# Kernel optimization log

Hardware: AMD Instinct MI355X
Metric: run time of the kernel (lower is better)

Reference implementation:

```python
import jax, jax.numpy as jnp
import numpy as np

H = 128
H1 = H + 1          # 129
FUSE = H1 * H1 * H1 # 2,146,689


def setup_inputs() -> dict:
    key = jax.random.key(0)
    ks = jax.random.split(key, 9)
    B = 64
    v = jax.random.normal(ks[0], (B, H), dtype=jnp.float32)
    a = jax.random.normal(ks[1], (B, H), dtype=jnp.float32)
    t = jax.random.normal(ks[2], (B, H), dtype=jnp.float32)
    # Linear params stored as [in, out]; xavier-ish scaling
    W1 = jax.random.normal(ks[3], (FUSE, H // 2), dtype=jnp.float32) * (1.0 / np.sqrt(FUSE))
    b1 = jnp.zeros((H // 2,), dtype=jnp.float32)
    W2 = jax.random.normal(ks[4], (H // 2, H // 4), dtype=jnp.float32) * (1.0 / np.sqrt(H // 2))
    b2 = jnp.zeros((H // 4,), dtype=jnp.float32)
    W3 = jax.random.normal(ks[5], (H // 4, 1), dtype=jnp.float32) * (1.0 / np.sqrt(H // 4))
    b3 = jnp.zeros((1,), dtype=jnp.float32)
    return {"v": v, "a": a, "t": t, "W1": W1, "b1": b1,
            "W2": W2, "b2": b2, "W3": W3, "b3": b3}


def reference(v, a, t, W1, b1, W2, b2, W3, b3):
    B = a.shape[0]
    one = jnp.ones((B, 1), dtype=a.dtype)
    a_h = jnp.concatenate([one, a], axis=1)  # [B, H+1]
    v_h = jnp.concatenate([one, v], axis=1)
    t_h = jnp.concatenate([one, t], axis=1)
    # triple outer product: fusion[b,i,j,k] = a_h[b,i]*v_h[b,j]*t_h[b,k]
    fusion = jnp.einsum('bi,bj,bk->bijk', a_h, v_h, t_h).reshape(B, -1)  # [B, (H+1)^3]
    # dropout p applied at eval is identity (torch Dropout in eval / p=0)
    y1 = jax.nn.relu(fusion @ W1 + b1)
    y2 = jax.nn.relu(y1 @ W2 + b2)
    return y2 @ W3 + b3  # [B, 1]
```

## Files before the change

kernel.cpp:

```cpp
#include <hip/hip_runtime.h>
#include <hip/hip_bf16.h>

#define H 128
#define H1 129
#define NSLAB (H1 * H1)
#define KP 164
#define NBLK 1024

typedef __attribute__((ext_vector_type(8))) short short8;
typedef __attribute__((ext_vector_type(4))) float float4v;
typedef __attribute__((ext_vector_type(2))) int int2v;
typedef __attribute__((ext_vector_type(4))) int int4v;

__device__ __forceinline__ unsigned short f2bf_bits(float x) {
    return __builtin_bit_cast(unsigned short, __float2bfloat16(x));
}
__device__ __forceinline__ unsigned packbf(float x, float y) {
    return (unsigned)f2bf_bits(x) | ((unsigned)f2bf_bits(y) << 16);
}

__global__ __launch_bounds__(256, 4) void k1_partial(
        const float* __restrict__ v, const float* __restrict__ a,
        const float* __restrict__ t, const float* __restrict__ W1,
        float* __restrict__ acc)
{
    __shared__ short lds[64 * KP];

    const int tid  = threadIdx.x;
    const int wv   = tid >> 6;
    const int lane = tid & 63;
    const int quad = lane >> 4;
    const int l15  = lane & 15;

    for (int idx = tid; idx < 64 * (KP - 130); idx += 256) {
        int n = idx / (KP - 130), k = 130 + idx % (KP - 130);
        lds[n * KP + k] = 0;
    }

    short8 tf[5];
    const int bt = 16 * wv + l15;
    #pragma unroll
    for (int s = 0; s < 5; ++s) {
        #pragma unroll
        for (int j = 0; j < 8; ++j) {
            int k = 32 * s + 8 * quad + j;
            float val = (k == 0) ? 1.0f : ((k <= H) ? t[bt * H + k - 1] : 0.0f);
            tf[s][j] = (short)f2bf_bits(val);
        }
    }

    const float4v vz = {0.f, 0.f, 0.f, 0.f};
    float4v y1acc[4] = {vz, vz, vz, vz};

    const int s0 = (int)(((long long)blockIdx.x * NSLAB) / NBLK);
    const int s1 = (int)(((long long)(blockIdx.x + 1) * NSLAB) / NBLK);
    int si = s0 / H1, sj = s0 % H1;

    const int q = tid & 15;
    const int p16 = tid >> 4;

    for (int sl = s0; sl < s1; ++sl) {
        const float* Wb = W1 + (long long)sl * (H1 * 64);

        float4v ra[4], rb[4];
        #pragma unroll
        for (int it = 0; it < 4; ++it) {
            int p = it * 16 + p16;
            ra[it] = *reinterpret_cast<const float4v*>(Wb + (2 * p) * 64 + q * 4);
            rb[it] = *reinterpret_cast<const float4v*>(Wb + (2 * p + 1) * 64 + q * 4);
        }
        float lastrow = 0.f;
        if (tid < 64) lastrow = Wb[128 * 64 + tid];

        #pragma unroll
        for (int it = 0; it < 4; ++it) {
            int p = it * 16 + p16;
            #pragma unroll
            for (int c = 0; c < 4; ++c) {
                int n = q * 4 + c;
                *reinterpret_cast<unsigned*>(&lds[n * KP + 2 * p]) = packbf(ra[it][c], rb[it][c]);
            }
        }
        if (tid < 64) {
            *reinterpret_cast<unsigned*>(&lds[tid * KP + 128]) = packbf(lastrow, 0.f);
        }
        __syncthreads();

        float4v avv;
        #pragma unroll
        for (int r = 0; r < 4; ++r) {
            int br = 16 * wv + quad * 4 + r;
            float ah = (si == 0) ? 1.0f : a[br * H + si - 1];
            float vh = (sj == 0) ? 1.0f : v[br * H + sj - 1];
            avv[r] = ah * vh;
        }

        float4v D[4] = {vz, vz, vz, vz};
        #pragma unroll
        for (int s = 0; s < 5; ++s) {
            #pragma unroll
            for (int nt = 0; nt < 4; ++nt) {
                int n = nt * 16 + l15;
                int sa = n * KP + 32 * s + 8 * quad;
                int2v lo = *reinterpret_cast<const int2v*>(&lds[sa]);
                int2v hi = *reinterpret_cast<const int2v*>(&lds[sa + 4]);
                int4v w; w.x = lo.x; w.y = lo.y; w.z = hi.x; w.w = hi.y;
                short8 bf = __builtin_bit_cast(short8, w);
                D[nt] = __builtin_amdgcn_mfma_f32_16x16x32_bf16(tf[s], bf, D[nt], 0, 0, 0);
            }
        }
        #pragma unroll
        for (int nt = 0; nt < 4; ++nt) y1acc[nt] += avv * D[nt];

        __syncthreads();

        ++sj; if (sj == H1) { sj = 0; ++si; }
    }

    #pragma unroll
    for (int nt = 0; nt < 4; ++nt) {
        int h = nt * 16 + l15;
        #pragma unroll
        for (int r = 0; r < 4; ++r) {
            int br = 16 * wv + quad * 4 + r;
            unsafeAtomicAdd(&acc[br * 64 + h], y1acc[nt][r]);
        }
    }
}

__global__ void k2_tail(const float* __restrict__ acc, const float* __restrict__ b1,
                        const float* __restrict__ W2, const float* __restrict__ b2,
                        const float* __restrict__ W3, const float* __restrict__ b3,
                        float* __restrict__ out)
{
    __shared__ float y1s[64 * 64];
    __shared__ float y2s[64 * 32];
    const int tid = threadIdx.x;

    for (int e = tid; e < 64 * 64; e += 256) {
        float x = acc[e] + b1[e & 63];
        y1s[e] = x > 0.f ? x : 0.f;
    }
    __syncthreads();
    for (int e = tid; e < 64 * 32; e += 256) {
        int b = e >> 5, h2 = e & 31;
        float s = b2[h2];
        #pragma unroll 8
        for (int h = 0; h < 64; ++h) s += y1s[b * 64 + h] * W2[h * 32 + h2];
        y2s[e] = s > 0.f ? s : 0.f;
    }
    __syncthreads();
    if (tid < 64) {
        float s = b3[0];
        #pragma unroll
        for (int h2 = 0; h2 < 32; ++h2) s += y2s[tid * 32 + h2] * W3[h2];
        out[tid] = s;
    }
}

extern "C" void kernel_launch(void* const* d_in, const int* in_sizes, int n_in,
                              void* d_out, int out_size, void* d_ws, size_t ws_size,
                              hipStream_t stream) {
    const float* v  = (const float*)d_in[0];
    const float* a  = (const float*)d_in[1];
    const float* t  = (const float*)d_in[2];
    const float* W1 = (const float*)d_in[3];
    const float* b1 = (const float*)d_in[4];
    const float* W2 = (const float*)d_in[5];
    const float* b2 = (const float*)d_in[6];
    const float* W3 = (const float*)d_in[7];
    const float* b3 = (const float*)d_in[8];
    float* acc = (float*)d_ws;

    hipMemsetAsync(acc, 0, 64 * 64 * sizeof(float), stream);
    hipLaunchKernelGGL(k1_partial, dim3(NBLK), dim3(256), 0, stream, v, a, t, W1, acc);
    hipLaunchKernelGGL(k2_tail, dim3(1), dim3(256), 0, stream,
                       acc, b1, W2, b2, W3, b3, (float*)d_out);
}
```

Baseline: 729.7 us.

## Drop LDS staging, register double-buffer W1 slabs, precompute a*v, reduce partials deterministically

The main kernel stops staging W1 through shared memory. Each lane now loads its W1 column elements straight into registers, with double buffering across slabs, and converts them to bf16 in place. The 129th t row is handled as a separate scalar FMA term, so the padded K slice goes away. A new pre-kernel writes all a*v products to workspace, and the per-block atomics are replaced by per-block partial sums plus a separate reduction kernel. Block count halves to 512, and launch bounds allow 2 blocks per CU. Risks are strided, uncoalesced global loads of W1 (each lane reads at a 64-float stride), extra workspace traffic for avf (about 4 MB) and the partials (8 MB), and two extra kernel launches.

```diff
diff --git a/kernel.cpp b/kernel.cpp
--- a/kernel.cpp
+++ b/kernel.cpp
@@ -4,131 +4,148 @@
 #define H 128
 #define H1 129
 #define NSLAB (H1 * H1)
-#define KP 164
-#define NBLK 1024
+#define SLABSZ (H1 * 64)
+#define NBLK 512
+#define AV_FLOATS (NSLAB * 64)
+#define PART_FLOATS (NBLK * 4096)
 
 typedef __attribute__((ext_vector_type(8))) short short8;
 typedef __attribute__((ext_vector_type(4))) float float4v;
-typedef __attribute__((ext_vector_type(2))) int int2v;
-typedef __attribute__((ext_vector_type(4))) int int4v;
-
-__device__ __forceinline__ unsigned short f2bf_bits(float x) {
-    return __builtin_bit_cast(unsigned short, __float2bfloat16(x));
-}
-__device__ __forceinline__ unsigned packbf(float x, float y) {
-    return (unsigned)f2bf_bits(x) | ((unsigned)f2bf_bits(y) << 16);
-}
-
-__global__ __launch_bounds__(256, 4) void k1_partial(
-        const float* __restrict__ v, const float* __restrict__ a,
+
+__device__ __forceinline__ short bfb(float x) {
+    return (short)__builtin_bit_cast(unsigned short, __float2bfloat16(x));
+}
+
+__global__ void k0_av(const float* __restrict__ a, const float* __restrict__ v,
+                      float* __restrict__ avf)
+{
+    int idx = blockIdx.x * 256 + threadIdx.x;
+    if (idx >= AV_FLOATS) return;
+    int sl = idx >> 6, b = idx & 63;
+    int si = sl / H1, sj = sl % H1;
+    float ah = (si == 0) ? 1.f : a[b * H + si - 1];
+    float vh = (sj == 0) ? 1.f : v[b * H + sj - 1];
+    avf[idx] = ah * vh;
+}
+
+__global__ __launch_bounds__(256, 2) void k1_partial(
         const float* __restrict__ t, const float* __restrict__ W1,
-        float* __restrict__ acc)
-{
-    __shared__ short lds[64 * KP];
-
+        const float* __restrict__ avf, float* __restrict__ partials)
+{
     const int tid  = threadIdx.x;
-    const int wv   = tid >> 6;
+    const int w    = tid >> 6;
     const int lane = tid & 63;
     const int quad = lane >> 4;
     const int l15  = lane & 15;
-
-    for (int idx = tid; idx < 64 * (KP - 130); idx += 256) {
-        int n = idx / (KP - 130), k = 130 + idx % (KP - 130);
-        lds[n * KP + k] = 0;
-    }
-
-    short8 tf[5];
-    const int bt = 16 * wv + l15;
+    const int ncol = 16 * w + l15;
+
+    short8 tf[4][4];
     #pragma unroll
-    for (int s = 0; s < 5; ++s) {
-        #pragma unroll
-        for (int j = 0; j < 8; ++j) {
-            int k = 32 * s + 8 * quad + j;
-            float val = (k == 0) ? 1.0f : ((k <= H) ? t[bt * H + k - 1] : 0.0f);
-            tf[s][j] = (short)f2bf_bits(val);
-        }
-    }
-
-    const float4v vz = {0.f, 0.f, 0.f, 0.f};
-    float4v y1acc[4] = {vz, vz, vz, vz};
+    for (int mt = 0; mt < 4; ++mt) {
+        int b = 16 * mt + l15;
+        #pragma unroll
+        for (int s = 0; s < 4; ++s) {
+            short8 f;
+            #pragma unroll
+            for (int j = 0; j < 8; ++j) {
+                int k = 32 * s + 8 * quad + j;
+                float val = (k == 0) ? 1.0f : t[b * H + k - 1];
+                f[j] = bfb(val);
+            }
+            tf[mt][s] = f;
+        }
+    }
+    float4v tl[4];
+    #pragma unroll
+    for (int mt = 0; mt < 4; ++mt)
+        #pragma unroll
+        for (int r = 0; r < 4; ++r)
+            tl[mt][r] = t[(16 * mt + 4 * quad + r) * H + 127];
 
     const int s0 = (int)(((long long)blockIdx.x * NSLAB) / NBLK);
     const int s1 = (int)(((long long)(blockIdx.x + 1) * NSLAB) / NBLK);
-    int si = s0 / H1, sj = s0 % H1;
-
-    const int q = tid & 15;
-    const int p16 = tid >> 4;
-
-    for (int sl = s0; sl < s1; ++sl) {
-        const float* Wb = W1 + (long long)sl * (H1 * 64);
-
-        float4v ra[4], rb[4];
-        #pragma unroll
-        for (int it = 0; it < 4; ++it) {
-            int p = it * 16 + p16;
-            ra[it] = *reinterpret_cast<const float4v*>(Wb + (2 * p) * 64 + q * 4);
-            rb[it] = *reinterpret_cast<const float4v*>(Wb + (2 * p + 1) * 64 + q * 4);
-        }
-        float lastrow = 0.f;
-        if (tid < 64) lastrow = Wb[128 * 64 + tid];
-
-        #pragma unroll
-        for (int it = 0; it < 4; ++it) {
-            int p = it * 16 + p16;
-            #pragma unroll
-            for (int c = 0; c < 4; ++c) {
-                int n = q * 4 + c;
-                *reinterpret_cast<unsigned*>(&lds[n * KP + 2 * p]) = packbf(ra[it][c], rb[it][c]);
-            }
-        }
-        if (tid < 64) {
-            *reinterpret_cast<unsigned*>(&lds[tid * KP + 128]) = packbf(lastrow, 0.f);
-        }
-        __syncthreads();
-
-        float4v avv;
-        #pragma unroll
-        for (int r = 0; r < 4; ++r) {
-            int br = 16 * wv + quad * 4 + r;
-            float ah = (si == 0) ? 1.0f : a[br * H + si - 1];
-            float vh = (sj == 0) ? 1.0f : v[br * H + sj - 1];
-            avv[r] = ah * vh;
-        }
-
+    const int niter = s1 - s0;
+
+    float   fb[2][4][8];
+    float4v avb[2][4];
+    float   wl[2];
+
+    auto LOADSLAB = [&](int sl, int p) __attribute__((always_inline)) {
+        const float* Wb = W1 + (long long)sl * SLABSZ;
+        #pragma unroll
+        for (int s = 0; s < 4; ++s) {
+            const float* rp = Wb + (32 * s + 8 * quad) * 64 + ncol;
+            #pragma unroll
+            for (int j = 0; j < 8; ++j) fb[p][s][j] = rp[j * 64];
+        }
+        wl[p] = Wb[128 * 64 + ncol];
+        const float* ap = avf + sl * 64 + 4 * quad;
+        #pragma unroll
+        for (int mt = 0; mt < 4; ++mt)
+            avb[p][mt] = *(const float4v*)(ap + 16 * mt);
+    };
+
+    const float4v vz = {0.f, 0.f, 0.f, 0.f};
+    float4v y1[4] = {vz, vz, vz, vz};
+
+    auto COMPUTE = [&](int p) __attribute__((always_inline)) {
         float4v D[4] = {vz, vz, vz, vz};
         #pragma unroll
-        for (int s = 0; s < 5; ++s) {
-            #pragma unroll
-            for (int nt = 0; nt < 4; ++nt) {
-                int n = nt * 16 + l15;
-                int sa = n * KP + 32 * s + 8 * quad;
-                int2v lo = *reinterpret_cast<const int2v*>(&lds[sa]);
-                int2v hi = *reinterpret_cast<const int2v*>(&lds[sa + 4]);
-                int4v w; w.x = lo.x; w.y = lo.y; w.z = hi.x; w.w = hi.y;
-                short8 bf = __builtin_bit_cast(short8, w);
-                D[nt] = __builtin_amdgcn_mfma_f32_16x16x32_bf16(tf[s], bf, D[nt], 0, 0, 0);
-            }
-        }
-        #pragma unroll
-        for (int nt = 0; nt < 4; ++nt) y1acc[nt] += avv * D[nt];
-
-        __syncthreads();
-
-        ++sj; if (sj == H1) { sj = 0; ++si; }
-    }
-
+        for (int s = 0; s < 4; ++s) {
+            short8 Bf;
+            #pragma unroll
+            for (int j = 0; j < 8; ++j) Bf[j] = bfb(fb[p][s][j]);
+            #pragma unroll
+            for (int mt = 0; mt < 4; ++mt)
+                D[mt] = __builtin_amdgcn_mfma_f32_16x16x32_bf16(tf[mt][s], Bf, D[mt], 0, 0, 0);
+        }
+        #pragma unroll
+        for (int mt = 0; mt < 4; ++mt) {
+            y1[mt] += avb[p][mt] * D[mt];
+            y1[mt] += (avb[p][mt] * tl[mt]) * wl[p];
+        }
+    };
+
+    LOADSLAB(s0, 0);
+    int it = 0;
+    for (; it + 2 <= niter; it += 2) {
+        int n1 = s0 + it + 1;
+        int n2 = (it + 2 < niter) ? s0 + it + 2 : s1 - 1;
+        LOADSLAB(n1, 1);
+        COMPUTE(0);
+        LOADSLAB(n2, 0);
+        COMPUTE(1);
+    }
+    if (it < niter) COMPUTE(0);
+
+    float* pp = partials + (long long)blockIdx.x * 4096;
     #pragma unroll
-    for (int nt = 0; nt < 4; ++nt) {
-        int h = nt * 16 + l15;
-        #pragma unroll
-        for (int r = 0; r < 4; ++r) {
-            int br = 16 * wv + quad * 4 + r;
-            unsafeAtomicAdd(&acc[br * 64 + h], y1acc[nt][r]);
-        }
-    }
-}
-
-__global__ void k2_tail(const float* __restrict__ acc, const float* __restrict__ b1,
+    for (int mt = 0; mt < 4; ++mt)
+        #pragma unroll
+        for (int r = 0; r < 4; ++r)
+            pp[(16 * mt + 4 * quad + r) * 64 + ncol] = y1[mt][r];
+}
+
+__global__ void k2_reduce(const float* __restrict__ partials, float* __restrict__ acc)
+{
+    __shared__ float red[8][32];
+    const int tid = threadIdx.x;
+    const int c = tid & 31, pg = tid >> 5;
+    const int cell = blockIdx.x * 32 + c;
+    float s = 0.f;
+    for (int p = pg; p < NBLK; p += 8)
+        s += partials[p * 4096 + cell];
+    red[pg][c] = s;
+    __syncthreads();
+    if (pg == 0) {
+        float tot = 0.f;
+        #pragma unroll
+        for (int g = 0; g < 8; ++g) tot += red[g][c];
+        acc[cell] = tot;
+    }
+}
+
+__global__ void k3_tail(const float* __restrict__ acc, const float* __restrict__ b1,
                         const float* __restrict__ W2, const float* __restrict__ b2,
                         const float* __restrict__ W3, const float* __restrict__ b3,
                         float* __restrict__ out)
@@ -170,10 +187,14 @@
     const float* b2 = (const float*)d_in[6];
     const float* W3 = (const float*)d_in[7];
     const float* b3 = (const float*)d_in[8];
-    float* acc = (float*)d_ws;
-
-    hipMemsetAsync(acc, 0, 64 * 64 * sizeof(float), stream);
-    hipLaunchKernelGGL(k1_partial, dim3(NBLK), dim3(256), 0, stream, v, a, t, W1, acc);
-    hipLaunchKernelGGL(k2_tail, dim3(1), dim3(256), 0, stream,
+
+    float* avf      = (float*)d_ws;
+    float* partials = avf + AV_FLOATS;
+    float* acc      = partials + PART_FLOATS;
+
+    hipLaunchKernelGGL(k0_av, dim3((AV_FLOATS + 255) / 256), dim3(256), 0, stream, a, v, avf);
+    hipLaunchKernelGGL(k1_partial, dim3(NBLK), dim3(256), 0, stream, t, W1, avf, partials);
+    hipLaunchKernelGGL(k2_reduce, dim3(128), dim3(256), 0, stream, partials, acc);
+    hipLaunchKernelGGL(k3_tail, dim3(1), dim3(256), 0, stream,
                        acc, b1, W2, b2, W3, b3, (float*)d_out);
 }
```

Result: slower. 755.7 us (+3.6%).
